# Optimization experiments

Measured on AMD Instinct MI355X. Metric: run time of the kernel, lower is better.

Reference implementation:

```python
import jax, jax.numpy as jnp
import numpy as np

ALPHA, GAMMA, THRESHOLD, NUM_CLASSES = 0.5, 1.5, 0.5, 21
EPS8, EPS7 = 1e-8, 1e-7


def corner_to_center(b):
    w = b[..., 2] - b[..., 0]
    h = b[..., 3] - b[..., 1]
    cx = b[..., 0] + w / 2
    cy = b[..., 1] + h / 2
    return jnp.stack([cx, cy, w, h], axis=-1)


def box_iou(b1, b2):
    # b1: [P,4], b2: [M,4] -> [P,M]
    area1 = (b1[:, 2] - b1[:, 0]) * (b1[:, 3] - b1[:, 1])
    area2 = (b2[:, 2] - b2[:, 0]) * (b2[:, 3] - b2[:, 1])
    lt = jnp.maximum(b1[:, None, :2], b2[None, :, :2])
    rb = jnp.minimum(b1[:, None, 2:], b2[None, :, 2:])
    wh = jnp.clip(rb - lt, 0)
    inter = wh[..., 0] * wh[..., 1]
    return inter / (area1[:, None] + area2[None, :] - inter)


def encode_boxes(matched, dbox):
    g = corner_to_center(matched)
    d = corner_to_center(dbox)
    ex = (g[..., 0] - d[..., 0]) / (d[..., 2] + EPS8)
    ey = (g[..., 1] - d[..., 1]) / (d[..., 3] + EPS8)
    ew = jnp.log(g[..., 2] / (d[..., 2] + EPS8) + EPS8)
    eh = jnp.log(g[..., 3] / (d[..., 3] + EPS8) + EPS8)
    return jnp.stack([ex, ey, ew, eh], axis=-1)


def decode_boxes(loc, dbox):
    d = corner_to_center(dbox)
    cx = loc[..., 0] * d[..., 2] + d[..., 0]
    cy = loc[..., 1] * d[..., 3] + d[..., 1]
    w = jnp.exp(loc[..., 2]) * d[..., 2]
    h = jnp.exp(loc[..., 3]) * d[..., 3]
    return jnp.stack([cx - w / 2, cy - h / 2, cx + w / 2, cy + h / 2], axis=-1)


def giou_loss(pred, tgt):
    inter_min = jnp.maximum(pred[..., :2], tgt[..., :2])
    inter_max = jnp.minimum(pred[..., 2:], tgt[..., 2:])
    inter_wh = jnp.clip(inter_max - inter_min, 0)
    inter = inter_wh[..., 0] * inter_wh[..., 1]
    pa = (pred[..., 2] - pred[..., 0]) * (pred[..., 3] - pred[..., 1])
    ta = (tgt[..., 2] - tgt[..., 0]) * (tgt[..., 3] - tgt[..., 1])
    union = pa + ta - inter
    iou = inter / (union + EPS7)
    encl_min = jnp.minimum(pred[..., :2], tgt[..., :2])
    encl_max = jnp.maximum(pred[..., 2:], tgt[..., 2:])
    encl_wh = jnp.clip(encl_max - encl_min, 0)
    encl = encl_wh[..., 0] * encl_wh[..., 1]
    giou = iou - (encl - union) / (encl + EPS7)
    return 1.0 - giou


def _match_one(truths, labels, dbox):
    # truths: [M,4], labels: [M], dbox: [P,4]
    M = truths.shape[0]
    overlaps = box_iou(dbox, truths)               # [P,M]
    bt_ov = overlaps.max(axis=1)                   # [P]
    bt_idx = overlaps.argmax(axis=1)               # [P]
    bp_idx = overlaps.argmax(axis=0)               # [M] best prior per GT
    # force-match each GT to its best prior
    bt_idx = bt_idx.at[bp_idx].set(jnp.arange(M))
    bt_ov = bt_ov.at[bp_idx].set(2.0)
    matches = truths[bt_idx]                       # [P,4]
    mlabels = jnp.where(bt_ov < THRESHOLD, 0, labels[bt_idx])
    loc_t = encode_boxes(matches, dbox)
    return loc_t, mlabels


def focal_loss(pred, target):
    # pred: [N,C], target: [N]
    logp = jax.nn.log_softmax(pred, axis=-1)
    ce = -jnp.take_along_axis(logp, target[:, None], axis=1)[:, 0]
    p_t = jnp.exp(-ce)
    return ALPHA * (1.0 - p_t) ** GAMMA * ce


def setup_inputs() -> dict:
    key = jax.random.key(0)
    k1, k2, k3, k4, k5, k6, k7 = jax.random.split(key, 7)
    B, P, M, C = 64, 24564, 50, 21
    # valid corner-format boxes: min + positive wh
    d_min = jax.random.uniform(k1, (P, 2)) * 0.8
    d_wh = 0.05 + jax.random.uniform(k2, (P, 2)) * 0.2
    default_boxes = jnp.concatenate([d_min, d_min + d_wh], axis=1)
    g_min = jax.random.uniform(k3, (B, M, 2)) * 0.8
    g_wh = 0.05 + jax.random.uniform(k4, (B, M, 2)) * 0.2
    gt_boxes = jnp.concatenate([g_min, g_min + g_wh], axis=2)
    loc_preds = jax.random.normal(k5, (B, P, 4)) * 0.1
    conf_preds = jax.random.normal(k6, (B, P, C))
    gt_labels = jax.random.randint(k7, (B, M), 1, C)
    return {"loc_preds": loc_preds, "conf_preds": conf_preds,
            "default_boxes": default_boxes, "gt_boxes": gt_boxes,
            "gt_labels": gt_labels}


def reference(loc_preds, conf_preds, default_boxes, gt_boxes, gt_labels):
    B, P, _ = loc_preds.shape
    loc_t, conf_t = jax.vmap(_match_one, in_axes=(0, 0, None))(gt_boxes, gt_labels, default_boxes)
    pos = conf_t > 0                                   # [B,P]
    num_pos = pos.sum()
    denom = jnp.maximum(num_pos, 1).astype(loc_preds.dtype)
    # localization: decode preds and targets against anchors, GIoU on positives
    decoded_pred = decode_boxes(loc_preds, default_boxes[None])
    decoded_tgt = decode_boxes(loc_t, default_boxes[None])
    gl = giou_loss(decoded_pred, decoded_tgt)          # [B,P]
    loc_loss = jnp.sum(jnp.where(pos, gl, 0.0)) / denom
    # classification: focal loss over all anchors
    fl = focal_loss(conf_preds.reshape(-1, conf_preds.shape[-1]), conf_t.reshape(-1))
    conf_loss = fl.sum() / denom
    total = loc_loss + conf_loss
    return jnp.where(num_pos == 0, 0.0, total)
```

## Files before the change

### kernel.cpp

```cpp
#include <hip/hip_runtime.h>
#include <cstdint>
#include <cstddef>

#define F_ALPHA 0.5f
#define THRESH  0.5f
#define EPS8    1e-8f
#define EPS7    1e-7f
#define MAXM    64
#define CCLS    21
#define GGRP    4
#define LOG2E   1.4426950408889634f
#define LN2     0.6931471805599453f

__global__ __launch_bounds__(256)
void bp_kernel(const float4* __restrict__ dbox,
               const float4* __restrict__ gt,
               unsigned* __restrict__ bp,
               float* __restrict__ garea,
               int P, int M)
{
    __shared__ unsigned long long wkey[GGRP][4];

    const int b  = blockIdx.y;
    const int m0 = blockIdx.x * GGRP;
    const int t  = threadIdx.x;
    const int w  = t >> 6, lane = t & 63;

    float4 gb[GGRP]; float ga[GGRP];
    #pragma unroll
    for (int g = 0; g < GGRP; g++) {
        int m = min(m0 + g, M - 1);
        float4 gg = gt[(size_t)b * M + m];
        gb[g] = gg;
        ga[g] = (gg.z - gg.x) * (gg.w - gg.y);
    }

    float    bestv[GGRP];
    unsigned bestp[GGRP];
    #pragma unroll
    for (int g = 0; g < GGRP; g++) { bestv[g] = 0.f; bestp[g] = 0u; }

    for (int p = t; p < P; p += 256) {
        float4 d = dbox[p];
        float darea = (d.z - d.x) * (d.w - d.y);
        #pragma unroll
        for (int g = 0; g < GGRP; g++) {
            float4 gg = gb[g];
            float lx = fmaxf(d.x, gg.x), ly = fmaxf(d.y, gg.y);
            float rx = fminf(d.z, gg.z), ry = fminf(d.w, gg.w);
            float iw = fmaxf(rx - lx, 0.f), ih = fmaxf(ry - ly, 0.f);
            float inter = iw * ih;
            float iou = inter * __builtin_amdgcn_rcpf(darea + ga[g] - inter);
            if (iou > bestv[g]) { bestv[g] = iou; bestp[g] = (unsigned)p; }
        }
    }

    #pragma unroll
    for (int g = 0; g < GGRP; g++) {
        unsigned long long k =
            ((unsigned long long)__float_as_uint(bestv[g]) << 32)
            | (unsigned long long)(0xFFFFFFFFu - bestp[g]);
        #pragma unroll
        for (int o = 1; o < 64; o <<= 1) {
            unsigned long long k2 = __shfl_xor(k, o, 64);
            if (k2 > k) k = k2;
        }
        if (lane == 0) wkey[g][w] = k;
    }
    __syncthreads();
    if (t < GGRP) {
        unsigned long long k0 = wkey[t][0], k1 = wkey[t][1];
        unsigned long long k2 = wkey[t][2], k3 = wkey[t][3];
        unsigned long long ka = (k0 > k1) ? k0 : k1;
        unsigned long long kb = (k2 > k3) ? k2 : k3;
        unsigned long long k  = (ka > kb) ? ka : kb;
        int m = m0 + t;
        if (m < M) {
            bp[(size_t)b * M + m] = 0xFFFFFFFFu - (unsigned)(k & 0xFFFFFFFFull);
            float4 gg = gt[(size_t)b * M + m];
            garea[(size_t)b * M + m] = (gg.z - gg.x) * (gg.w - gg.y);
        }
    }
}

__global__ __launch_bounds__(256, 6)
void loss_kernel(const float4* __restrict__ locp,
                 const float*  __restrict__ conf,
                 const float4* __restrict__ dbox,
                 const float4* __restrict__ gt,
                 const float*  __restrict__ garea,
                 const int*    __restrict__ gtl,
                 const unsigned* __restrict__ bp,
                 double* __restrict__ partS,
                 int*    __restrict__ partC,
                 int P, int M)
{
    __shared__ float    scf[256 * CCLS];
    __shared__ float4   tb[MAXM];
    __shared__ int      tl[MAXM];
    __shared__ int      ovr[256];
    __shared__ double   sv[4];
    __shared__ int      sc[4];

    const int t = threadIdx.x;
    const int b = blockIdx.y;
    const int p0 = blockIdx.x * 256;
    const int p = p0 + t;
    const bool valid = (p < P);

    ovr[t] = -1;
    if (t < M) {
        tb[t] = gt[(size_t)b * M + t];
        tl[t] = gtl[(size_t)b * M + t];
    }

    const int cnt = min(256, P - p0);
    const int nf = cnt * CCLS;
    const float* src = conf + ((size_t)b * P + p0) * CCLS;
    {
        const int n4 = nf >> 2;
        const float4* s4 = (const float4*)src;
        float4* d4 = (float4*)scf;
        for (int i = t; i < n4; i += 256) d4[i] = s4[i];
        for (int i = (n4 << 2) + t; i < nf; i += 256) scf[i] = src[i];
    }
    __syncthreads();

    if (t < M) {
        unsigned q = bp[(size_t)b * M + t] - (unsigned)p0;
        if (q < 256u) atomicMax(&ovr[q], t);
    }

    float4 d = make_float4(0.f, 0.f, 0.f, 0.f);
    float bi = -1.0f, bd = 1.0f;
    int   bm = 0;
    if (valid) {
        d = dbox[p];
        const float darea = (d.z - d.x) * (d.w - d.y);
        const float4* gtb = gt + (size_t)b * M;
        const float*  gab = garea + (size_t)b * M;
        #pragma unroll 4
        for (int m = 0; m < M; m++) {
            float4 g = gtb[m];
            float ta = gab[m];
            float lx = fmaxf(d.x, g.x), ly = fmaxf(d.y, g.y);
            float rx = fminf(d.z, g.z), ry = fminf(d.w, g.w);
            float iw = fmaxf(rx - lx, 0.f), ih = fmaxf(ry - ly, 0.f);
            float inter = iw * ih;
            float den = darea + ta - inter;
            if (inter * bd > bi * den) { bi = inter; bd = den; bm = m; }
        }
    }
    __syncthreads();

    double acc = 0.0;
    int cnt_pos = 0;
    if (valid) {
        int  idx = bm;
        bool pos = (bi >= THRESH * bd);
        { int j = ovr[t]; if (j >= 0) { idx = j; pos = true; } }
        int lbl = pos ? tl[idx] : 0;

        float xv[CCLS];
        const float* x = scf + t * CCLS;
        #pragma unroll
        for (int c = 0; c < CCLS; c++) xv[c] = x[c];
        float xl = scf[t * CCLS + lbl];
        float mx = xv[0];
        #pragma unroll
        for (int c = 1; c < CCLS; c++) mx = fmaxf(mx, xv[c]);
        float h = mx * LOG2E;
        float sum = 0.f;
        #pragma unroll
        for (int c = 0; c < CCLS; c++)
            sum += __builtin_exp2f(__builtin_fmaf(xv[c], LOG2E, -h));
        float ce = (mx + __builtin_log2f(sum) * LN2) - xl;
        float pt = __builtin_exp2f(-ce * LOG2E);
        float om = 1.f - pt;
        acc = (double)(F_ALPHA * om * __builtin_sqrtf(om) * ce);

        if (pos) {
            cnt_pos = 1;
            float dw = d.z - d.x, dh = d.w - d.y;
            float dcx = d.x + dw * 0.5f, dcy = d.y + dh * 0.5f;
            float4 g = tb[idx];
            float gw = g.z - g.x, gh = g.w - g.y;
            float gcx = g.x + gw * 0.5f, gcy = g.y + gh * 0.5f;
            float ex = (gcx - dcx) / (dw + EPS8);
            float ey = (gcy - dcy) / (dh + EPS8);
            float ew = logf(gw / (dw + EPS8) + EPS8);
            float eh = logf(gh / (dh + EPS8) + EPS8);
            float tcx = ex * dw + dcx, tcy = ey * dh + dcy;
            float tw = expf(ew) * dw,  th = expf(eh) * dh;
            float t0 = tcx - tw * 0.5f, t1 = tcy - th * 0.5f;
            float t2 = tcx + tw * 0.5f, t3 = tcy + th * 0.5f;
            float4 l = locp[(size_t)b * P + p];
            float pcx = l.x * dw + dcx, pcy = l.y * dh + dcy;
            float pw = expf(l.z) * dw,  ph = expf(l.w) * dh;
            float q0 = pcx - pw * 0.5f, q1 = pcy - ph * 0.5f;
            float q2 = pcx + pw * 0.5f, q3 = pcy + ph * 0.5f;
            float ix0 = fmaxf(q0, t0), iy0 = fmaxf(q1, t1);
            float ix1 = fminf(q2, t2), iy1 = fminf(q3, t3);
            float iw = fmaxf(ix1 - ix0, 0.f), ih = fmaxf(iy1 - iy0, 0.f);
            float inter = iw * ih;
            float pa = (q2 - q0) * (q3 - q1);
            float ta = (t2 - t0) * (t3 - t1);
            float uni = pa + ta - inter;
            float iou = inter / (uni + EPS7);
            float e0 = fminf(q0, t0), e1 = fminf(q1, t1);
            float e2 = fmaxf(q2, t2), e3 = fmaxf(q3, t3);
            float ewd = fmaxf(e2 - e0, 0.f), ehd = fmaxf(e3 - e1, 0.f);
            float encl = ewd * ehd;
            float giou = iou - (encl - uni) / (encl + EPS7);
            acc += (double)(1.f - giou);
        }
    }

    for (int o = 32; o > 0; o >>= 1) {
        acc += __shfl_down(acc, o, 64);
        cnt_pos += __shfl_down(cnt_pos, o, 64);
    }
    int w = t >> 6, lane = t & 63;
    if (lane == 0) { sv[w] = acc; sc[w] = cnt_pos; }
    __syncthreads();
    if (t == 0) {
        int slot = blockIdx.y * gridDim.x + blockIdx.x;
        partS[slot] = sv[0] + sv[1] + sv[2] + sv[3];
        partC[slot] = sc[0] + sc[1] + sc[2] + sc[3];
    }
}

__global__ __launch_bounds__(256)
void final_kernel(const double* __restrict__ partS,
                  const int*    __restrict__ partC,
                  float* __restrict__ out, int n)
{
    __shared__ double sv[4];
    __shared__ long long sc[4];
    const int t = threadIdx.x;
    double a = 0.0; long long c = 0;
    for (int i = t; i < n; i += 256) { a += partS[i]; c += partC[i]; }
    for (int o = 32; o > 0; o >>= 1) {
        a += __shfl_down(a, o, 64);
        c += __shfl_down(c, o, 64);
    }
    int w = t >> 6, lane = t & 63;
    if (lane == 0) { sv[w] = a; sc[w] = c; }
    __syncthreads();
    if (t == 0) {
        double s = sv[0] + sv[1] + sv[2] + sv[3];
        long long np = sc[0] + sc[1] + sc[2] + sc[3];
        out[0] = (np == 0) ? 0.0f : (float)(s / (double)np);
    }
}

extern "C" void kernel_launch(void* const* d_in, const int* in_sizes, int n_in,
                              void* d_out, int out_size, void* d_ws, size_t ws_size,
                              hipStream_t stream)
{
    const float* locp = (const float*)d_in[0];
    const float* conf = (const float*)d_in[1];
    const float* dbox = (const float*)d_in[2];
    const float* gt   = (const float*)d_in[3];
    const int*   gtl  = (const int*)d_in[4];

    const int P  = in_sizes[2] / 4;
    const long long BP = (long long)in_sizes[0] / 4;
    const int B  = (int)(BP / P);
    const int M  = in_sizes[4] / B;

    const int nblk = (P + 255) / 256;
    const int nPart = nblk * B;

    char* ws = (char*)d_ws;
    unsigned* bp = (unsigned*)ws;
    size_t off = ((size_t)B * M * 4 + 15) & ~(size_t)15;
    float* garea = (float*)(ws + off);
    off += ((size_t)B * M * 4 + 15) & ~(size_t)15;
    double* partS = (double*)(ws + off);
    off += (size_t)nPart * 8;
    int* partC = (int*)(ws + off);

    dim3 gridBP((M + GGRP - 1) / GGRP, B);
    dim3 grid(nblk, B);
    bp_kernel<<<gridBP, 256, 0, stream>>>((const float4*)dbox, (const float4*)gt,
                                          bp, garea, P, M);
    loss_kernel<<<grid, 256, 0, stream>>>((const float4*)locp, conf,
                                          (const float4*)dbox, (const float4*)gt,
                                          garea, gtl, bp, partS, partC, P, M);
    final_kernel<<<1, 256, 0, stream>>>(partS, partC, (float*)d_out, nPart);
}
```

Measured before the change: 298.5 us.

## Process two anchors per thread and read conf rows directly from global

Each thread now handles two anchors, so every ground-truth box load in the matching loop serves two IoU evaluations, and the block count is halved. The shared-memory staging of confidence logits is removed; each thread reads its own 21-float row with unaligned 16-byte loads, which lowers LDS usage but makes the global accesses strided and uncoalesced. Divisions, log and exp in the GIoU path are replaced by hardware reciprocal and exp2/log2 builtins, and the launch-bounds occupancy hint drops from 6 to 4.

```diff
diff --git a/kernel.cpp b/kernel.cpp
--- a/kernel.cpp
+++ b/kernel.cpp
@@ -11,6 +11,12 @@
 #define GGRP    4
 #define LOG2E   1.4426950408889634f
 #define LN2     0.6931471805599453f
+
+__device__ __forceinline__ float4 ldg4u(const float* p) {
+    float4 v;
+    __builtin_memcpy(&v, p, 16);
+    return v;
+}
 
 __global__ __launch_bounds__(256)
 void bp_kernel(const float4* __restrict__ dbox,
@@ -83,7 +89,88 @@
     }
 }
 
-__global__ __launch_bounds__(256, 6)
+__device__ __forceinline__ void anchor_loss(
+    bool valid, float4 d, float bi, float bd, int bm, int ov,
+    const int* __restrict__ tl, const float4* __restrict__ tb,
+    const float* confRow, const float4* locpP,
+    double& acc, int& cnt_pos)
+{
+    if (!valid) return;
+
+    int  idx = bm;
+    bool pos = (bi >= THRESH * bd);
+    if (ov >= 0) { idx = ov; pos = true; }
+    const int lbl = pos ? tl[idx] : 0;
+
+    float xv[CCLS];
+    float4 v0 = ldg4u(confRow +  0);
+    float4 v1 = ldg4u(confRow +  4);
+    float4 v2 = ldg4u(confRow +  8);
+    float4 v3 = ldg4u(confRow + 12);
+    float4 v4 = ldg4u(confRow + 16);
+    xv[0]=v0.x;  xv[1]=v0.y;  xv[2]=v0.z;  xv[3]=v0.w;
+    xv[4]=v1.x;  xv[5]=v1.y;  xv[6]=v1.z;  xv[7]=v1.w;
+    xv[8]=v2.x;  xv[9]=v2.y;  xv[10]=v2.z; xv[11]=v2.w;
+    xv[12]=v3.x; xv[13]=v3.y; xv[14]=v3.z; xv[15]=v3.w;
+    xv[16]=v4.x; xv[17]=v4.y; xv[18]=v4.z; xv[19]=v4.w;
+    xv[20]=confRow[20];
+    float xl = confRow[lbl];
+
+    float mx = xv[0];
+    #pragma unroll
+    for (int c = 1; c < CCLS; c++) mx = fmaxf(mx, xv[c]);
+    float h = mx * LOG2E;
+    float sum = 0.f;
+    #pragma unroll
+    for (int c = 0; c < CCLS; c++)
+        sum += __builtin_exp2f(__builtin_fmaf(xv[c], LOG2E, -h));
+    float ce = (mx + __builtin_log2f(sum) * LN2) - xl;
+    float pt = __builtin_exp2f(-ce * LOG2E);
+    float om = 1.f - pt;
+    acc += (double)(F_ALPHA * om * __builtin_sqrtf(om) * ce);
+
+    if (pos) {
+        cnt_pos += 1;
+        float dw = d.z - d.x, dh = d.w - d.y;
+        float dcx = d.x + dw * 0.5f, dcy = d.y + dh * 0.5f;
+        float4 g = tb[idx];
+        float gw = g.z - g.x, gh = g.w - g.y;
+        float gcx = g.x + gw * 0.5f, gcy = g.y + gh * 0.5f;
+        float rdw = __builtin_amdgcn_rcpf(dw + EPS8);
+        float rdh = __builtin_amdgcn_rcpf(dh + EPS8);
+        float ex = (gcx - dcx) * rdw;
+        float ey = (gcy - dcy) * rdh;
+        float ew = __builtin_log2f(gw * rdw + EPS8) * LN2;
+        float eh = __builtin_log2f(gh * rdh + EPS8) * LN2;
+        float tcx = ex * dw + dcx, tcy = ey * dh + dcy;
+        float tw = __builtin_exp2f(ew * LOG2E) * dw;
+        float th = __builtin_exp2f(eh * LOG2E) * dh;
+        float t0 = tcx - tw * 0.5f, t1 = tcy - th * 0.5f;
+        float t2 = tcx + tw * 0.5f, t3 = tcy + th * 0.5f;
+        float4 l = *locpP;
+        float pcx = l.x * dw + dcx, pcy = l.y * dh + dcy;
+        float pw = __builtin_exp2f(l.z * LOG2E) * dw;
+        float ph = __builtin_exp2f(l.w * LOG2E) * dh;
+        float q0 = pcx - pw * 0.5f, q1 = pcy - ph * 0.5f;
+        float q2 = pcx + pw * 0.5f, q3 = pcy + ph * 0.5f;
+        float ix0 = fmaxf(q0, t0), iy0 = fmaxf(q1, t1);
+        float ix1 = fminf(q2, t2), iy1 = fminf(q3, t3);
+        float iw = fmaxf(ix1 - ix0, 0.f), ih = fmaxf(iy1 - iy0, 0.f);
+        float inter = iw * ih;
+        float pa = (q2 - q0) * (q3 - q1);
+        float ta = (t2 - t0) * (t3 - t1);
+        float uni = pa + ta - inter;
+        float iou = inter * __builtin_amdgcn_rcpf(uni + EPS7);
+        float e0 = fminf(q0, t0), e1 = fminf(q1, t1);
+        float e2 = fmaxf(q2, t2), e3 = fmaxf(q3, t3);
+        float ewd = fmaxf(e2 - e0, 0.f), ehd = fmaxf(e3 - e1, 0.f);
+        float encl = ewd * ehd;
+        float giou = iou - (encl - uni) * __builtin_amdgcn_rcpf(encl + EPS7);
+        acc += (double)(1.f - giou);
+    }
+}
+
+__global__ __launch_bounds__(256, 4)
 void loss_kernel(const float4* __restrict__ locp,
                  const float*  __restrict__ conf,
                  const float4* __restrict__ dbox,
@@ -95,126 +182,71 @@
                  int*    __restrict__ partC,
                  int P, int M)
 {
-    __shared__ float    scf[256 * CCLS];
-    __shared__ float4   tb[MAXM];
-    __shared__ int      tl[MAXM];
-    __shared__ int      ovr[256];
-    __shared__ double   sv[4];
-    __shared__ int      sc[4];
-
-    const int t = threadIdx.x;
-    const int b = blockIdx.y;
-    const int p0 = blockIdx.x * 256;
-    const int p = p0 + t;
-    const bool valid = (p < P);
-
-    ovr[t] = -1;
+    __shared__ float4 tb[MAXM];
+    __shared__ int    tl[MAXM];
+    __shared__ int    ovr[512];
+    __shared__ double sv[4];
+    __shared__ int    sc[4];
+
+    const int t  = threadIdx.x;
+    const int b  = blockIdx.y;
+    const int p0 = blockIdx.x * 512;
+    const int pA = p0 + t;
+    const int pB = p0 + 256 + t;
+    const bool validA = (pA < P);
+    const bool validB = (pB < P);
+
+    ovr[t] = -1; ovr[t + 256] = -1;
     if (t < M) {
         tb[t] = gt[(size_t)b * M + t];
         tl[t] = gtl[(size_t)b * M + t];
     }
-
-    const int cnt = min(256, P - p0);
-    const int nf = cnt * CCLS;
-    const float* src = conf + ((size_t)b * P + p0) * CCLS;
-    {
-        const int n4 = nf >> 2;
-        const float4* s4 = (const float4*)src;
-        float4* d4 = (float4*)scf;
-        for (int i = t; i < n4; i += 256) d4[i] = s4[i];
-        for (int i = (n4 << 2) + t; i < nf; i += 256) scf[i] = src[i];
-    }
     __syncthreads();
 
     if (t < M) {
         unsigned q = bp[(size_t)b * M + t] - (unsigned)p0;
-        if (q < 256u) atomicMax(&ovr[q], t);
-    }
-
-    float4 d = make_float4(0.f, 0.f, 0.f, 0.f);
-    float bi = -1.0f, bd = 1.0f;
-    int   bm = 0;
-    if (valid) {
-        d = dbox[p];
-        const float darea = (d.z - d.x) * (d.w - d.y);
-        const float4* gtb = gt + (size_t)b * M;
-        const float*  gab = garea + (size_t)b * M;
-        #pragma unroll 4
-        for (int m = 0; m < M; m++) {
-            float4 g = gtb[m];
-            float ta = gab[m];
-            float lx = fmaxf(d.x, g.x), ly = fmaxf(d.y, g.y);
-            float rx = fminf(d.z, g.z), ry = fminf(d.w, g.w);
+        if (q < 512u) atomicMax(&ovr[q], t);
+    }
+
+    const float4 dA = dbox[validA ? pA : (P - 1)];
+    const float4 dB = dbox[validB ? pB : (P - 1)];
+    const float daA = (dA.z - dA.x) * (dA.w - dA.y);
+    const float daB = (dB.z - dB.x) * (dB.w - dB.y);
+    const float4* gtb = gt + (size_t)b * M;
+    const float*  gab = garea + (size_t)b * M;
+    float biA = -1.f, bdA = 1.f, biB = -1.f, bdB = 1.f;
+    int   bmA = 0, bmB = 0;
+    #pragma unroll 2
+    for (int m = 0; m < M; m++) {
+        float4 g = gtb[m];
+        float ta = gab[m];
+        {
+            float lx = fmaxf(dA.x, g.x), ly = fmaxf(dA.y, g.y);
+            float rx = fminf(dA.z, g.z), ry = fminf(dA.w, g.w);
             float iw = fmaxf(rx - lx, 0.f), ih = fmaxf(ry - ly, 0.f);
             float inter = iw * ih;
-            float den = darea + ta - inter;
-            if (inter * bd > bi * den) { bi = inter; bd = den; bm = m; }
+            float den = daA + ta - inter;
+            if (inter * bdA > biA * den) { biA = inter; bdA = den; bmA = m; }
+        }
+        {
+            float lx = fmaxf(dB.x, g.x), ly = fmaxf(dB.y, g.y);
+            float rx = fminf(dB.z, g.z), ry = fminf(dB.w, g.w);
+            float iw = fmaxf(rx - lx, 0.f), ih = fmaxf(ry - ly, 0.f);
+            float inter = iw * ih;
+            float den = daB + ta - inter;
+            if (inter * bdB > biB * den) { biB = inter; bdB = den; bmB = m; }
         }
     }
     __syncthreads();
 
     double acc = 0.0;
     int cnt_pos = 0;
-    if (valid) {
-        int  idx = bm;
-        bool pos = (bi >= THRESH * bd);
-        { int j = ovr[t]; if (j >= 0) { idx = j; pos = true; } }
-        int lbl = pos ? tl[idx] : 0;
-
-        float xv[CCLS];
-        const float* x = scf + t * CCLS;
-        #pragma unroll
-        for (int c = 0; c < CCLS; c++) xv[c] = x[c];
-        float xl = scf[t * CCLS + lbl];
-        float mx = xv[0];
-        #pragma unroll
-        for (int c = 1; c < CCLS; c++) mx = fmaxf(mx, xv[c]);
-        float h = mx * LOG2E;
-        float sum = 0.f;
-        #pragma unroll
-        for (int c = 0; c < CCLS; c++)
-            sum += __builtin_exp2f(__builtin_fmaf(xv[c], LOG2E, -h));
-        float ce = (mx + __builtin_log2f(sum) * LN2) - xl;
-        float pt = __builtin_exp2f(-ce * LOG2E);
-        float om = 1.f - pt;
-        acc = (double)(F_ALPHA * om * __builtin_sqrtf(om) * ce);
-
-        if (pos) {
-            cnt_pos = 1;
-            float dw = d.z - d.x, dh = d.w - d.y;
-            float dcx = d.x + dw * 0.5f, dcy = d.y + dh * 0.5f;
-            float4 g = tb[idx];
-            float gw = g.z - g.x, gh = g.w - g.y;
-            float gcx = g.x + gw * 0.5f, gcy = g.y + gh * 0.5f;
-            float ex = (gcx - dcx) / (dw + EPS8);
-            float ey = (gcy - dcy) / (dh + EPS8);
-            float ew = logf(gw / (dw + EPS8) + EPS8);
-            float eh = logf(gh / (dh + EPS8) + EPS8);
-            float tcx = ex * dw + dcx, tcy = ey * dh + dcy;
-            float tw = expf(ew) * dw,  th = expf(eh) * dh;
-            float t0 = tcx - tw * 0.5f, t1 = tcy - th * 0.5f;
-            float t2 = tcx + tw * 0.5f, t3 = tcy + th * 0.5f;
-            float4 l = locp[(size_t)b * P + p];
-            float pcx = l.x * dw + dcx, pcy = l.y * dh + dcy;
-            float pw = expf(l.z) * dw,  ph = expf(l.w) * dh;
-            float q0 = pcx - pw * 0.5f, q1 = pcy - ph * 0.5f;
-            float q2 = pcx + pw * 0.5f, q3 = pcy + ph * 0.5f;
-            float ix0 = fmaxf(q0, t0), iy0 = fmaxf(q1, t1);
-            float ix1 = fminf(q2, t2), iy1 = fminf(q3, t3);
-            float iw = fmaxf(ix1 - ix0, 0.f), ih = fmaxf(iy1 - iy0, 0.f);
-            float inter = iw * ih;
-            float pa = (q2 - q0) * (q3 - q1);
-            float ta = (t2 - t0) * (t3 - t1);
-            float uni = pa + ta - inter;
-            float iou = inter / (uni + EPS7);
-            float e0 = fminf(q0, t0), e1 = fminf(q1, t1);
-            float e2 = fmaxf(q2, t2), e3 = fmaxf(q3, t3);
-            float ewd = fmaxf(e2 - e0, 0.f), ehd = fmaxf(e3 - e1, 0.f);
-            float encl = ewd * ehd;
-            float giou = iou - (encl - uni) / (encl + EPS7);
-            acc += (double)(1.f - giou);
-        }
-    }
+    const size_t bP = (size_t)b * P;
+    anchor_loss(validA, dA, biA, bdA, bmA, ovr[t], tl, tb,
+                conf + (bP + pA) * CCLS, locp + bP + pA, acc, cnt_pos);
+    anchor_loss(validB, dB, biB, bdB, bmB, ovr[t + 256], tl, tb,
+                conf + (bP + (validB ? pB : 0)) * CCLS,
+                locp + bP + (validB ? pB : 0), acc, cnt_pos);
 
     for (int o = 32; o > 0; o >>= 1) {
         acc += __shfl_down(acc, o, 64);
@@ -269,7 +301,7 @@
     const int B  = (int)(BP / P);
     const int M  = in_sizes[4] / B;
 
-    const int nblk = (P + 255) / 256;
+    const int nblk = (P + 511) / 512;
     const int nPart = nblk * B;
 
     char* ws = (char*)d_ws;
```

Measured after the change: 294.8 us. No clear change (-1.2%).
